# Optimization experiments

Measured on AMD Instinct MI355X. Metric: run time of the kernel, lower is better.

Reference implementation:

```python
import jax, jax.numpy as jnp
import numpy as np

V, H, L, S, B = 32000, 1024, 4, 256, 16


def setup_inputs() -> dict:
    key = jax.random.key(0)
    ks = jax.random.split(key, 6)
    s = 0.02  # init scale
    return {
        "x": jax.random.randint(ks[0], (S, B), 0, V, dtype=jnp.int32),
        "h0": jnp.zeros((L, B, H), jnp.float32),
        "c0": jnp.zeros((L, B, H), jnp.float32),
        "emb": jax.random.normal(ks[1], (V, H), jnp.float32) * s,
        "W_ih": jax.random.normal(ks[2], (L, 4 * H, H), jnp.float32) * s,
        "W_hh": jax.random.normal(ks[3], (L, 4 * H, H), jnp.float32) * s,
        "b_ih": jnp.zeros((L, 4 * H), jnp.float32),
        "b_hh": jnp.zeros((L, 4 * H), jnp.float32),
        "fc_W": jax.random.normal(ks[4], (V, H), jnp.float32) * s,
        "fc_b": jnp.zeros((V,), jnp.float32),
    }


def _lstm_layer(xs, h0, c0, Wih, Whh, b):
    # xs: [S, B, Hin]; torch gate order is (i, f, g, o)
    def step(carry, x_t):
        h, c = carry
        z = x_t @ Wih.T + h @ Whh.T + b  # [B, 4H]
        i, f, g, o = jnp.split(z, 4, axis=-1)
        c = jax.nn.sigmoid(f) * c + jax.nn.sigmoid(i) * jnp.tanh(g)
        h = jax.nn.sigmoid(o) * jnp.tanh(c)
        return (h, c), h

    (hT, cT), ys = jax.lax.scan(step, (h0, c0), xs)
    return ys, hT, cT


def reference(x, h0, c0, emb, W_ih, W_hh, b_ih, b_hh, fc_W, fc_b):
    y = emb[x]  # [S, B, H]
    h_fin, c_fin = [], []
    for l in range(L):  # fixed small layer count; time dim handled by scan
        y, hT, cT = _lstm_layer(y, h0[l], c0[l], W_ih[l], W_hh[l], b_ih[l] + b_hh[l])
        h_fin.append(hT)
        c_fin.append(cT)
    logits = y @ fc_W.T + fc_b  # [S, B, V]
    return logits, jnp.stack(h_fin), jnp.stack(c_fin)
```

## Files before the change

kernel.cpp:

```cpp
#include <hip/hip_runtime.h>
#include <hip/hip_bf16.h>

typedef unsigned short u16;
typedef short short8 __attribute__((ext_vector_type(8)));
typedef u16 u16x8 __attribute__((ext_vector_type(8)));
typedef float f32x4 __attribute__((ext_vector_type(4)));

#define H 1024
#define NB 16
#define SEQ 256
#define NL 4
#define VOCAB 32000
#define G4 4096
#define YSZ ((size_t)SEQ * NB * H)

__device__ __forceinline__ u16 f2bf(float f) {
  __hip_bfloat16 h = __float2bfloat16(f);
  return *reinterpret_cast<u16*>(&h);
}
__device__ __forceinline__ float sigm(float x) { return 1.0f / (1.0f + __expf(-x)); }
__device__ __forceinline__ float tanhfast(float x) { return 2.0f / (1.0f + __expf(-2.0f * x)) - 1.0f; }

__device__ __forceinline__ f32x4 mfma16(short8 a, short8 b, f32x4 c) {
  return __builtin_amdgcn_mfma_f32_16x16x32_bf16(a, b, c, 0, 0, 0);
}

template <int BOFF>
__device__ __forceinline__ short8 ldg_sc(const u16* p) {
  short8 r;
  asm volatile("global_load_dwordx4 %0, %1, off offset:%2 sc0 sc1"
               : "=&v"(r) : "v"(p), "n"(BOFF));
  return r;
}

#define WAITV0                                                 \
  do {                                                         \
    asm volatile("s_waitcnt vmcnt(0)" ::: "memory");           \
    __builtin_amdgcn_sched_barrier(0);                         \
  } while (0)

#define LD8SC(d, p)                                            \
  do {                                                         \
    d[0] = ldg_sc<0 * 64>(p); d[1] = ldg_sc<1 * 64>(p);        \
    d[2] = ldg_sc<2 * 64>(p); d[3] = ldg_sc<3 * 64>(p);        \
    d[4] = ldg_sc<4 * 64>(p); d[5] = ldg_sc<5 * 64>(p);        \
    d[6] = ldg_sc<6 * 64>(p); d[7] = ldg_sc<7 * 64>(p);        \
  } while (0)


__global__ void cvt_bf16(const float* __restrict__ in, u16* __restrict__ out, int n8) {
  const int i = blockIdx.x * blockDim.x + threadIdx.x;
  if (i >= n8) return;
  const float4 a = ((const float4*)in)[2 * i];
  const float4 b = ((const float4*)in)[2 * i + 1];
  u16x8 o;
  o[0] = f2bf(a.x); o[1] = f2bf(a.y); o[2] = f2bf(a.z); o[3] = f2bf(a.w);
  o[4] = f2bf(b.x); o[5] = f2bf(b.y); o[6] = f2bf(b.z); o[7] = f2bf(b.w);
  *(u16x8*)(out + (size_t)i * 8) = o;
}

__global__ void bias_sum(const float* __restrict__ a, const float* __restrict__ b,
                         float* __restrict__ o, int n) {
  const int i = blockIdx.x * blockDim.x + threadIdx.x;
  if (i < n) o[i] = a[i] + b[i];
}

__global__ void zero_u32(unsigned* __restrict__ p, int n) {
  const int i = blockIdx.x * blockDim.x + threadIdx.x;
  if (i < n) p[i] = 0u;
}

__global__ void gather_emb(const int* __restrict__ x, const float* __restrict__ emb,
                           u16* __restrict__ Y) {
  const int row = blockIdx.x;
  const int tok = x[row];
  const float4 v = ((const float4*)(emb + (size_t)tok * H))[threadIdx.x];
  ushort4 o;
  o.x = f2bf(v.x); o.y = f2bf(v.y); o.z = f2bf(v.z); o.w = f2bf(v.w);
  *(ushort4*)(Y + (size_t)row * H + threadIdx.x * 4) = o;
}

__device__ __forceinline__ void wavewait(const unsigned* __restrict__ base, unsigned tgt) {
  const unsigned* p = base + (threadIdx.x & 63) * 16;
  unsigned v;
  do {
    asm volatile("global_load_dword %0, %1, off sc0 sc1\n\ts_waitcnt vmcnt(0)"
                 : "=&v"(v) : "v"(p) : "memory");
  } while (!__all(v >= tgt));
  __builtin_amdgcn_sched_barrier(0);
}


__global__ __launch_bounds__(256, 1) void lstm_scan(
    const u16* __restrict__ ybase_r, u16* __restrict__ ybase_w,
    const u16* __restrict__ Wih_all, const u16* __restrict__ Whh_all,
    const float* __restrict__ bias_all, const u16* __restrict__ h0_all,
    const float* __restrict__ c0_all, float* __restrict__ hfin_all,
    float* __restrict__ cfin_all, unsigned* __restrict__ bars)
{
  extern __shared__ u16 sm[];
  u16* __restrict__ smw = sm;
  f32x4* __restrict__ lred = (f32x4*)(sm + 65536);
  u16* __restrict__ smh = sm + 73728;

  const int tid = threadIdx.x;
  const int lane = tid & 63;
  const int wid = tid >> 6;
  const int l = blockIdx.x >> 6;
  const int jgrp = blockIdx.x & 63;
  const int jbase = jgrp * 16;
  const int b = lane & 15;
  const int lg = lane >> 4;
  const int m = lane & 15;
  const int j = jbase + wid * 4 + lg;

  const u16* __restrict__ Yin  = ybase_r + (size_t)l * YSZ;
  u16* __restrict__ Yout       = ybase_w + (size_t)(l + 1) * YSZ;
  const u16* __restrict__ Wih  = Wih_all + (size_t)l * G4 * H;
  const u16* __restrict__ Whh  = Whh_all + (size_t)l * G4 * H;
  const float* __restrict__ bias = bias_all + (size_t)l * G4;
  const u16* __restrict__ h0b  = h0_all + (size_t)l * NB * H;
  const float* __restrict__ c0 = c0_all + (size_t)l * NB * H;
  float* __restrict__ hfin     = hfin_all + (size_t)l * NB * H;
  float* __restrict__ cfin     = cfin_all + (size_t)l * NB * H;
  unsigned* __restrict__ myflags = bars + l * 1024;
  const unsigned* __restrict__ xflags = bars + (l - 1) * 1024;
  unsigned* __restrict__ myflag_wr = myflags + jgrp * 16;

  #pragma unroll
  for (int rt = 0; rt < 4; ++rt) {
    const size_t ar = (size_t)((m & 3) * H + jbase + rt * 4 + (m >> 2));
    const u16* src = Whh + ar * H + lg * 8;
    #pragma unroll
    for (int i = 0; i < 8; ++i) {
      const int ks = wid * 8 + i;
      short8 w = *(const short8*)(src + ks * 32);
      *(short8*)(smw + (size_t)rt * 16384 + (size_t)ks * 512 + lane * 8) = w;
    }
  }
  short8 WI[32];
  #pragma unroll
  for (int rt = 0; rt < 4; ++rt) {
    const size_t ar = (size_t)((m & 3) * H + jbase + rt * 4 + (m >> 2));
    const u16* src = Wih + ar * H + lg * 8;
    #pragma unroll
    for (int i = 0; i < 8; ++i) {
      WI[rt * 8 + i] = *(const short8*)(src + (wid * 8 + i) * 32);
      asm volatile("" : "+v"(WI[rt * 8 + i]));
    }
  }
  __syncthreads();

  f32x4 bias4;
  bias4[0] = bias[0 * H + j];
  bias4[1] = bias[1 * H + j];
  bias4[2] = bias[2 * H + j];
  bias4[3] = bias[3 * H + j];

  float c = c0[b * H + j];
  const int boff = b * H + lg * 8;
  const int kboff = wid * 256;
  const u16* __restrict__ smwv = smw + (size_t)wid * 4096 + lane * 8;

  for (int t = 0; t < SEQ; ++t) {
    const u16* xw = Yin + (size_t)t * (NB * H) + boff + kboff;

    f32x4 a0 = {0.f, 0.f, 0.f, 0.f};
    f32x4 a1 = {0.f, 0.f, 0.f, 0.f};
    f32x4 a2 = {0.f, 0.f, 0.f, 0.f};
    f32x4 a3 = {0.f, 0.f, 0.f, 0.f};

    short8 fx[8];
    if (l == 0) {
      #pragma unroll
      for (int i = 0; i < 8; ++i) fx[i] = *(const short8*)(xw + i * 32);
    } else {
      wavewait(xflags, (unsigned)(t + 1));
      LD8SC(fx, xw);
      WAITV0;
    }
    #pragma unroll
    for (int i = 0; i < 8; ++i) {
      a0 = mfma16(WI[0 * 8 + i], fx[i], a0);
      a1 = mfma16(WI[1 * 8 + i], fx[i], a1);
      a2 = mfma16(WI[2 * 8 + i], fx[i], a2);
      a3 = mfma16(WI[3 * 8 + i], fx[i], a3);
    }

    short8 fh[8];
    if (t == 0) {
      const u16* hw = h0b + boff + kboff;
      #pragma unroll
      for (int i = 0; i < 8; ++i) fh[i] = *(const short8*)(hw + i * 32);
    } else {
      const u16* hw = Yout + (size_t)(t - 1) * (NB * H) + boff + kboff;
      wavewait(myflags, (unsigned)t);
      LD8SC(fh, hw);
      WAITV0;
    }
    #pragma unroll
    for (int i = 0; i < 8; ++i) {
      short8 w0 = *(const short8*)(smwv + 0 * 16384 + i * 512);
      short8 w1 = *(const short8*)(smwv + 1 * 16384 + i * 512);
      short8 w2 = *(const short8*)(smwv + 2 * 16384 + i * 512);
      short8 w3 = *(const short8*)(smwv + 3 * 16384 + i * 512);
      a0 = mfma16(w0, fh[i], a0);
      a1 = mfma16(w1, fh[i], a1);
      a2 = mfma16(w2, fh[i], a2);
      a3 = mfma16(w3, fh[i], a3);
    }

    if (wid != 0) lred[(0 * 4 + wid) * 64 + lane] = a0;
    if (wid != 1) lred[(1 * 4 + wid) * 64 + lane] = a1;
    if (wid != 2) lred[(2 * 4 + wid) * 64 + lane] = a2;
    if (wid != 3) lred[(3 * 4 + wid) * 64 + lane] = a3;
    __syncthreads();

    f32x4 z4 = bias4;
    if (wid == 0)      z4 += a0;
    else if (wid == 1) z4 += a1;
    else if (wid == 2) z4 += a2;
    else               z4 += a3;
    #pragma unroll
    for (int w2 = 0; w2 < 4; ++w2)
      if (w2 != wid) z4 += lred[(wid * 4 + w2) * 64 + lane];

    const float ig = sigm(z4[0]);
    const float fg = sigm(z4[1]);
    const float gg = tanhfast(z4[2]);
    const float og = sigm(z4[3]);
    c = fg * c + ig * gg;
    const float h = og * tanhfast(c);

    smh[b * 16 + wid * 4 + lg] = f2bf(h);
    if (t == SEQ - 1) {
      hfin[b * H + j] = h;
      cfin[b * H + j] = c;
    }

    __syncthreads();
    if (wid == 0) {
      if (lane < 32) {
        const int br = lane >> 1, half = lane & 1;
        u16x8 pv = *(const u16x8*)&smh[br * 16 + half * 8];
        const u16* dst = Yout + (size_t)t * (NB * H) + (size_t)br * H + jbase + half * 8;
        asm volatile("global_store_dwordx4 %0, %1, off sc0 sc1"
                     :: "v"(dst), "v"(pv) : "memory");
      }
      asm volatile("s_waitcnt vmcnt(0)" ::: "memory");
      if (lane == 0) {
        const unsigned tv = (unsigned)(t + 1);
        asm volatile("global_store_dword %0, %1, off sc0 sc1"
                     :: "v"(myflag_wr), "v"(tv) : "memory");
      }
    }
  }
}


__global__ __launch_bounds__(256, 1) void gemm_bt_bias(
    const u16* __restrict__ A, const u16* __restrict__ Bw,
    const float* __restrict__ bias, float* __restrict__ C, int N)
{
  __shared__ u16 As[128 * 64];
  __shared__ u16 Bs[128 * 64];
  const int tid = threadIdx.x;
  const int lane = tid & 63;
  const int wid = tid >> 6;
  const int m0 = blockIdx.x * 128;
  const int n0 = blockIdx.y * 128;
  const int wr = wid >> 1, wc = wid & 1;
  const int lr = lane >> 3;
  const int lc = (lane & 7) * 8;
  f32x4 acc[4][4] = {};

  for (int k0 = 0; k0 < H; k0 += 64) {
    __syncthreads();
    #pragma unroll
    for (int cc = 0; cc < 4; ++cc) {
      const int row = wid * 32 + cc * 8 + lr;
      __builtin_amdgcn_global_load_lds(
          (const __attribute__((address_space(1))) void*)(A + (size_t)(m0 + row) * H + k0 + lc),
          (__attribute__((address_space(3))) void*)(As + row * 64 + lc), 16, 0, 0);
      __builtin_amdgcn_global_load_lds(
          (const __attribute__((address_space(1))) void*)(Bw + (size_t)(n0 + row) * H + k0 + lc),
          (__attribute__((address_space(3))) void*)(Bs + row * 64 + lc), 16, 0, 0);
    }
    __syncthreads();
    #pragma unroll
    for (int ks = 0; ks < 2; ++ks) {
      short8 af[4], bfr[4];
      #pragma unroll
      for (int i = 0; i < 4; ++i) {
        af[i]  = *(const short8*)&As[(wr * 64 + i * 16 + (lane & 15)) * 64 + ks * 32 + (lane >> 4) * 8];
        bfr[i] = *(const short8*)&Bs[(wc * 64 + i * 16 + (lane & 15)) * 64 + ks * 32 + (lane >> 4) * 8];
      }
      #pragma unroll
      for (int i = 0; i < 4; ++i) {
        #pragma unroll
        for (int jj = 0; jj < 4; ++jj)
          acc[i][jj] = mfma16(af[i], bfr[jj], acc[i][jj]);
      }
    }
  }

  #pragma unroll
  for (int jj = 0; jj < 4; ++jj) {
    const int col = n0 + wc * 64 + jj * 16 + (lane & 15);
    const float bv = bias[col];
    #pragma unroll
    for (int i = 0; i < 4; ++i) {
      const int rbase = m0 + wr * 64 + i * 16 + (lane >> 4) * 4;
      #pragma unroll
      for (int r = 0; r < 4; ++r)
        C[(size_t)(rbase + r) * N + col] = acc[i][jj][r] + bv;
    }
  }
}


extern "C" void kernel_launch(void* const* d_in, const int* in_sizes, int n_in,
                              void* d_out, int out_size, void* d_ws, size_t ws_size,
                              hipStream_t stream) {
  const int*   x    = (const int*)d_in[0];
  const float* h0   = (const float*)d_in[1];
  const float* c0   = (const float*)d_in[2];
  const float* emb  = (const float*)d_in[3];
  const float* W_ih = (const float*)d_in[4];
  const float* W_hh = (const float*)d_in[5];
  const float* b_ih = (const float*)d_in[6];
  const float* b_hh = (const float*)d_in[7];
  const float* fc_W = (const float*)d_in[8];
  const float* fc_b = (const float*)d_in[9];
  float* out = (float*)d_out;
  char* ws = (char*)d_ws;

  size_t off = 0;
  u16* WihB = (u16*)(ws + off); off += (size_t)NL * G4 * H * 2;
  u16* WhhB = (u16*)(ws + off); off += (size_t)NL * G4 * H * 2;
  u16* fcWB = (u16*)(ws + off); off += (size_t)VOCAB * H * 2;
  u16* h0B  = (u16*)(ws + off); off += (size_t)NL * NB * H * 2;
  float* biasB = (float*)(ws + off); off += (size_t)NL * G4 * 4;
  u16* ybufs = (u16*)(ws + off); off += (size_t)(NL + 1) * YSZ * 2;
  unsigned* bars = (unsigned*)(ws + off); off += 16384;
  if (ws_size < off) return;

  int n8;
  n8 = NL * G4 * H / 8;  cvt_bf16<<<(n8 + 255) / 256, 256, 0, stream>>>(W_ih, WihB, n8);
  n8 = NL * G4 * H / 8;  cvt_bf16<<<(n8 + 255) / 256, 256, 0, stream>>>(W_hh, WhhB, n8);
  n8 = VOCAB * H / 8;    cvt_bf16<<<(n8 + 255) / 256, 256, 0, stream>>>(fc_W, fcWB, n8);
  n8 = NL * NB * H / 8;  cvt_bf16<<<(n8 + 255) / 256, 256, 0, stream>>>(h0, h0B, n8);
  bias_sum<<<(NL * G4 + 255) / 256, 256, 0, stream>>>(b_ih, b_hh, biasB, NL * G4);
  zero_u32<<<16, 256, 0, stream>>>(bars, 4096);
  gather_emb<<<SEQ * NB, 256, 0, stream>>>(x, emb, ybufs);

  float* hfin = out + (size_t)SEQ * NB * VOCAB;
  float* cfin = hfin + (size_t)NL * NB * H;

  lstm_scan<<<NL * 64, 256, 147968, stream>>>(
      ybufs, ybufs, WihB, WhhB, biasB, h0B, c0, hfin, cfin, bars);

  gemm_bt_bias<<<dim3(32, 250), 256, 0, stream>>>(
      ybufs + (size_t)NL * YSZ, fcWB, fc_b, out, VOCAB);
}
```

Baseline: 1.709 ms.

## Merge x/h flag polling, compact flags, stream W_ih from global memory

Replaces the two separate per-wave flag waits with one combined poll over a compacted 64-entry-per-layer flag array. After the poll, the x and h inputs are read with plain loads instead of cache-bypassing sc0/sc1 loads. W_ih is no longer held in 128 VGPRs; each step re-reads it from global memory. This aims to cut polling round trips and register pressure, but it serializes the input projection behind the recurrent dependency and adds per-step weight traffic. Plain loads of data written by other blocks may also read stale cached values.

After: 4.063 ms. +137.7%, slower.

```diff
diff --git a/kernel.cpp b/kernel.cpp
--- a/kernel.cpp
+++ b/kernel.cpp
@@ -24,28 +24,6 @@
 __device__ __forceinline__ f32x4 mfma16(short8 a, short8 b, f32x4 c) {
   return __builtin_amdgcn_mfma_f32_16x16x32_bf16(a, b, c, 0, 0, 0);
 }
-
-template <int BOFF>
-__device__ __forceinline__ short8 ldg_sc(const u16* p) {
-  short8 r;
-  asm volatile("global_load_dwordx4 %0, %1, off offset:%2 sc0 sc1"
-               : "=&v"(r) : "v"(p), "n"(BOFF));
-  return r;
-}
-
-#define WAITV0                                                 \
-  do {                                                         \
-    asm volatile("s_waitcnt vmcnt(0)" ::: "memory");           \
-    __builtin_amdgcn_sched_barrier(0);                         \
-  } while (0)
-
-#define LD8SC(d, p)                                            \
-  do {                                                         \
-    d[0] = ldg_sc<0 * 64>(p); d[1] = ldg_sc<1 * 64>(p);        \
-    d[2] = ldg_sc<2 * 64>(p); d[3] = ldg_sc<3 * 64>(p);        \
-    d[4] = ldg_sc<4 * 64>(p); d[5] = ldg_sc<5 * 64>(p);        \
-    d[6] = ldg_sc<6 * 64>(p); d[7] = ldg_sc<7 * 64>(p);        \
-  } while (0)
 
 
 __global__ void cvt_bf16(const float* __restrict__ in, u16* __restrict__ out, int n8) {
@@ -80,13 +58,15 @@
   *(ushort4*)(Y + (size_t)row * H + threadIdx.x * 4) = o;
 }
 
-__device__ __forceinline__ void wavewait(const unsigned* __restrict__ base, unsigned tgt) {
-  const unsigned* p = base + (threadIdx.x & 63) * 16;
-  unsigned v;
+__device__ __forceinline__ void pollboth(const unsigned* __restrict__ xp, unsigned xt,
+                                         const unsigned* __restrict__ hp, unsigned ht) {
+  unsigned xv, hv;
   do {
-    asm volatile("global_load_dword %0, %1, off sc0 sc1\n\ts_waitcnt vmcnt(0)"
-                 : "=&v"(v) : "v"(p) : "memory");
-  } while (!__all(v >= tgt));
+    asm volatile("global_load_dword %0, %2, off sc0 sc1\n\t"
+                 "global_load_dword %1, %3, off sc0 sc1\n\t"
+                 "s_waitcnt vmcnt(0)"
+                 : "=&v"(xv), "=&v"(hv) : "v"(xp), "v"(hp) : "memory");
+  } while (!__all(xv >= xt && hv >= ht));
   __builtin_amdgcn_sched_barrier(0);
 }
 
@@ -123,9 +103,9 @@
   const float* __restrict__ c0 = c0_all + (size_t)l * NB * H;
   float* __restrict__ hfin     = hfin_all + (size_t)l * NB * H;
   float* __restrict__ cfin     = cfin_all + (size_t)l * NB * H;
-  unsigned* __restrict__ myflags = bars + l * 1024;
-  const unsigned* __restrict__ xflags = bars + (l - 1) * 1024;
-  unsigned* __restrict__ myflag_wr = myflags + jgrp * 16;
+  const unsigned* __restrict__ xflag_p = bars + (l > 0 ? (l - 1) : 0) * 64 + lane;
+  const unsigned* __restrict__ hflag_p = bars + l * 64 + lane;
+  unsigned* __restrict__ myflag_wr = bars + l * 64 + jgrp;
 
   #pragma unroll
   for (int rt = 0; rt < 4; ++rt) {
@@ -138,17 +118,10 @@
       *(short8*)(smw + (size_t)rt * 16384 + (size_t)ks * 512 + lane * 8) = w;
     }
   }
-  short8 WI[32];
-  #pragma unroll
-  for (int rt = 0; rt < 4; ++rt) {
-    const size_t ar = (size_t)((m & 3) * H + jbase + rt * 4 + (m >> 2));
-    const u16* src = Wih + ar * H + lg * 8;
-    #pragma unroll
-    for (int i = 0; i < 8; ++i) {
-      WI[rt * 8 + i] = *(const short8*)(src + (wid * 8 + i) * 32);
-      asm volatile("" : "+v"(WI[rt * 8 + i]));
-    }
-  }
+  const u16* __restrict__ wr0 = Wih + (size_t)((m & 3) * H + jbase + 0 * 4 + (m >> 2)) * H + (wid * 8) * 32 + lg * 8;
+  const u16* __restrict__ wr1 = Wih + (size_t)((m & 3) * H + jbase + 1 * 4 + (m >> 2)) * H + (wid * 8) * 32 + lg * 8;
+  const u16* __restrict__ wr2 = Wih + (size_t)((m & 3) * H + jbase + 2 * 4 + (m >> 2)) * H + (wid * 8) * 32 + lg * 8;
+  const u16* __restrict__ wr3 = Wih + (size_t)((m & 3) * H + jbase + 3 * 4 + (m >> 2)) * H + (wid * 8) * 32 + lg * 8;
   __syncthreads();
 
   f32x4 bias4;
@@ -163,40 +136,30 @@
   const u16* __restrict__ smwv = smw + (size_t)wid * 4096 + lane * 8;
 
   for (int t = 0; t < SEQ; ++t) {
+    const unsigned xt = (l > 0) ? (unsigned)(t + 1) : 0u;
+    const unsigned ht = (unsigned)t;
+    if ((xt | ht) != 0u) pollboth(xflag_p, xt, hflag_p, ht);
+
     const u16* xw = Yin + (size_t)t * (NB * H) + boff + kboff;
+    const u16* hw = (t == 0 ? h0b : Yout + (size_t)(t - 1) * (NB * H)) + boff + kboff;
+
+    short8 fx[8], fh[8];
+    #pragma unroll
+    for (int i = 0; i < 8; ++i) fx[i] = *(const short8*)(xw + i * 32);
+    #pragma unroll
+    for (int i = 0; i < 8; ++i) fh[i] = *(const short8*)(hw + i * 32);
 
     f32x4 a0 = {0.f, 0.f, 0.f, 0.f};
     f32x4 a1 = {0.f, 0.f, 0.f, 0.f};
     f32x4 a2 = {0.f, 0.f, 0.f, 0.f};
     f32x4 a3 = {0.f, 0.f, 0.f, 0.f};
 
-    short8 fx[8];
-    if (l == 0) {
-      #pragma unroll
-      for (int i = 0; i < 8; ++i) fx[i] = *(const short8*)(xw + i * 32);
-    } else {
-      wavewait(xflags, (unsigned)(t + 1));
-      LD8SC(fx, xw);
-      WAITV0;
-    }
     #pragma unroll
     for (int i = 0; i < 8; ++i) {
-      a0 = mfma16(WI[0 * 8 + i], fx[i], a0);
-      a1 = mfma16(WI[1 * 8 + i], fx[i], a1);
-      a2 = mfma16(WI[2 * 8 + i], fx[i], a2);
-      a3 = mfma16(WI[3 * 8 + i], fx[i], a3);
-    }
-
-    short8 fh[8];
-    if (t == 0) {
-      const u16* hw = h0b + boff + kboff;
-      #pragma unroll
-      for (int i = 0; i < 8; ++i) fh[i] = *(const short8*)(hw + i * 32);
-    } else {
-      const u16* hw = Yout + (size_t)(t - 1) * (NB * H) + boff + kboff;
-      wavewait(myflags, (unsigned)t);
-      LD8SC(fh, hw);
-      WAITV0;
+      a0 = mfma16(*(const short8*)(wr0 + i * 32), fx[i], a0);
+      a1 = mfma16(*(const short8*)(wr1 + i * 32), fx[i], a1);
+      a2 = mfma16(*(const short8*)(wr2 + i * 32), fx[i], a2);
+      a3 = mfma16(*(const short8*)(wr3 + i * 32), fx[i], a3);
     }
     #pragma unroll
     for (int i = 0; i < 8; ++i) {
@@ -351,7 +314,7 @@
   n8 = VOCAB * H / 8;    cvt_bf16<<<(n8 + 255) / 256, 256, 0, stream>>>(fc_W, fcWB, n8);
   n8 = NL * NB * H / 8;  cvt_bf16<<<(n8 + 255) / 256, 256, 0, stream>>>(h0, h0B, n8);
   bias_sum<<<(NL * G4 + 255) / 256, 256, 0, stream>>>(b_ih, b_hh, biasB, NL * G4);
-  zero_u32<<<16, 256, 0, stream>>>(bars, 4096);
+  zero_u32<<<4, 256, 0, stream>>>(bars, 1024);
   gather_emb<<<SEQ * NB, 256, 0, stream>>>(x, emb, ybufs);
 
   float* hfin = out + (size_t)SEQ * NB * VOCAB;
```
